# Kernel optimization log

Hardware: AMD Instinct MI355X
Metric: run time of the kernel (lower is better)

Reference implementation:

```python
import jax, jax.numpy as jnp
import numpy as np

H_SIZE, Z_SIZE, A_SIZE, INTER = 50, 100, 2, 100
T = 16384
SLOPE = 0.01  # torch leaky_relu default


def _lrelu(x):
    return jnp.where(x >= 0, x, SLOPE * x)


def setup_inputs() -> dict:
    key = jax.random.key(0)
    ks = jax.random.split(key, 20)
    s = 0.05
    inp = {
        "z_seq": jax.random.normal(ks[0], (T, 1, Z_SIZE), jnp.float32),
        "a_seq": jax.random.normal(ks[1], (T, 1, A_SIZE), jnp.float32),
        "term_seq": jax.random.uniform(ks[2], (T, 1, 1), jnp.float32),
        "W1": jax.random.normal(ks[3], (100, Z_SIZE + A_SIZE)) * s,
        "b1": jnp.zeros((100,), jnp.float32),
        "W2": jax.random.normal(ks[4], (INTER, 100)) * s,
        "b2": jnp.zeros((INTER,), jnp.float32),
        "W3": jax.random.normal(ks[5], (100, INTER)) * s,
        "b3": jnp.zeros((100,), jnp.float32),
        "W4": jax.random.normal(ks[6], (H_SIZE, 100)) * s,
        "b4": jnp.zeros((H_SIZE,), jnp.float32),
        "W5": jax.random.normal(ks[7], (100, INTER + H_SIZE)) * s,
        "b5": jnp.zeros((100,), jnp.float32),
        "Wz": jax.random.normal(ks[8], (Z_SIZE, 100)) * s,
        "bz": jnp.zeros((Z_SIZE,), jnp.float32),
        "Wt": jax.random.normal(ks[9], (1, 100)) * s,
        "bt": jnp.zeros((1,), jnp.float32),
    }
    return inp


def reference(z_seq, a_seq, term_seq, W1, b1, W2, b2, W3, b3, W4, b4, W5, b5, Wz, bz, Wt, bt):
    def step(h, xs):
        a, z, z_next, term_next = xs  # a:[1,2] z:[1,100] term_next:[1,1]
        # encode_az
        az = jnp.concatenate([a, z], axis=1)  # [1,102]
        inter = _lrelu(az @ W1.T + b1)
        inter = _lrelu(inter @ W2.T + b2)
        # update_h (residual)
        h = h + (_lrelu(inter @ W3.T + b3) @ W4.T + b4)
        # predict_output
        inp = jnp.concatenate([h, inter], axis=1)  # [1,150]
        i5 = _lrelu(inp @ W5.T + b5)
        z_pred = i5 @ Wz.T + bz
        t_logit = i5 @ Wt.T + bt
        z_loss = jnp.mean((z_next - z_pred) ** 2)
        # BCE with logits (stable)
        t_loss = jnp.mean(jnp.maximum(t_logit, 0) - t_logit * term_next
                          + jnp.log1p(jnp.exp(-jnp.abs(t_logit))))
        return h, (z_loss, t_loss)

    h0 = jnp.zeros((1, H_SIZE), z_seq.dtype)
    _, (zl, tl) = jax.lax.scan(
        step, h0, (a_seq[:-1], z_seq[:-1], z_seq[1:], term_seq[1:]))
    z_loss = jnp.mean(zl)
    term_loss = jnp.mean(tl)
    return (z_loss + term_loss, z_loss, term_loss)
```

## Files before the change

kernel.cpp:

```cpp
#include <hip/hip_runtime.h>
#include <math.h>

#define NS   16383
#define NSP  16384
#define LPB  32
#define NBLK 512
#define TPB  512

#define OFF_INTR 0
#define OFF_DELT (OFF_INTR + 1048576)
#define OFF_CSUM (OFF_DELT + 819200)
#define OFF_BZ   (OFF_CSUM + 50*NBLK)
#define OFF_BT   (OFF_BZ + NBLK)
#define OFF_PACK (OFF_BT + NBLK)

#define PK1 0
#define PK2 16384
#define PK3 32768
#define PK4 49152
#define PK5 57344
#define PKZ 81920
#define PKTOT 98304

using bf16x8 = __attribute__((ext_vector_type(8))) short;
using f32x4  = __attribute__((ext_vector_type(4))) float;

__device__ __forceinline__ unsigned short f2bf(float f) {
    unsigned int x = __float_as_uint(f);
    return (unsigned short)((x + 0x7fffu + ((x >> 16) & 1u)) >> 16);
}
__device__ __forceinline__ float bf2f(unsigned short u) {
    return __uint_as_float(((unsigned int)u) << 16);
}
__device__ __forceinline__ float lrelu(float x) { return fmaxf(x, 0.01f * x); }

__device__ __forceinline__ bf16x8 ldA(const unsigned short* buf, int strideSh, int row, int kc) {
    const int idx = (row * strideSh + kc) ^ ((row & 7) << 3);
    return *(const bf16x8*)(buf + idx);
}
__device__ __forceinline__ bf16x8 ldB(const unsigned short* pk, int KS, int nt, int ks, int lane) {
    return *(const bf16x8*)(pk + (size_t)(((nt * KS + ks) << 6) + lane) * 8);
}
__device__ __forceinline__ f32x4 MF(bf16x8 a, bf16x8 b, f32x4 c) {
    return __builtin_amdgcn_mfma_f32_16x16x32_bf16(a, b, c, 0, 0, 0);
}

#define MLAYER(INBUF, PKOFF, KSN, BIAS, OUTBUF)                                 \
    {                                                                           \
        const int nn = w * 16 + rl;                                             \
        const float bv = (nn < 100) ? (BIAS)[nn] : 0.f;                         \
        bf16x8 bfr[KSN];                                                        \
        _Pragma("unroll")                                                       \
        for (int ks = 0; ks < (KSN); ++ks)                                      \
            bfr[ks] = ldB(packw + (PKOFF), KSN, w, ks, lane);                   \
        _Pragma("unroll")                                                       \
        for (int m = 0; m < 2; ++m) {                                           \
            f32x4 acc; acc.x = bv; acc.y = bv; acc.z = bv; acc.w = bv;          \
            _Pragma("unroll")                                                   \
            for (int ks = 0; ks < (KSN); ++ks)                                  \
                acc = MF(ldA(INBUF, 128, m * 16 + rl, ks * 32 + g8), bfr[ks], acc); \
            _Pragma("unroll")                                                   \
            for (int r = 0; r < 4; ++r) {                                       \
                const int row = m * 16 + dr + r;                                \
                (OUTBUF)[((row << 7) + nn) ^ ((row & 7) << 3)] = f2bf(lrelu(acc[r])); \
            }                                                                   \
        }                                                                       \
    }

__global__ __launch_bounds__(256)
void k0_pack(const float* __restrict__ W1, const float* __restrict__ W2,
             const float* __restrict__ W3, const float* __restrict__ W4,
             const float* __restrict__ W5, const float* __restrict__ Wz,
             float* __restrict__ ws)
{
    const int idx = blockIdx.x * 256 + threadIdx.x;
    if (idx >= PKTOT) return;
    int e, KS, layer;
    if      (idx < PK2) { layer = 1; e = idx - PK1; KS = 4; }
    else if (idx < PK3) { layer = 2; e = idx - PK2; KS = 4; }
    else if (idx < PK4) { layer = 3; e = idx - PK3; KS = 4; }
    else if (idx < PK5) { layer = 4; e = idx - PK4; KS = 4; }
    else if (idx < PKZ) { layer = 5; e = idx - PK5; KS = 6; }
    else                { layer = 6; e = idx - PKZ; KS = 4; }
    const int j    = e & 7;
    const int ln   = (e >> 3) & 63;
    const int rest = e >> 9;
    const int ks   = rest % KS;
    const int nt   = rest / KS;
    const int n    = nt * 16 + (ln & 15);
    const int k    = ks * 32 + ((ln >> 4) << 3) + j;
    float v = 0.f;
    if (layer == 1)      { if (n < 100 && k < 102) v = W1[n * 102 + k]; }
    else if (layer == 2) { if (n < 100 && k < 100) v = W2[n * 100 + k]; }
    else if (layer == 3) { if (n < 100 && k < 100) v = W3[n * 100 + k]; }
    else if (layer == 4) { if (n < 50  && k < 100) v = W4[n * 100 + k]; }
    else if (layer == 5) { if (n < 100) {
                               if (k < 50) v = W5[n * 150 + k];
                               else if (k >= 64 && k < 164) v = W5[n * 150 + k - 14]; } }
    else                 { if (n < 100 && k < 100) v = Wz[n * 100 + k]; }
    ((unsigned short*)(ws + OFF_PACK))[idx] = f2bf(v);
}

__global__ __launch_bounds__(TPB, 4)
void k1_encode(const float* __restrict__ z_seq, const float* __restrict__ a_seq,
               const float* __restrict__ b1, const float* __restrict__ b2,
               const float* __restrict__ b3, const float* __restrict__ b4,
               float* __restrict__ ws)
{
    __shared__ unsigned short Vp[32 * 128];
    __shared__ unsigned short Vq[32 * 128];
    __shared__ float Dl[32 * 64];

    const int tid  = threadIdx.x;
    const int lane = tid & 63;
    const int w    = __builtin_amdgcn_readfirstlane(tid >> 6);
    const int blk  = blockIdx.x;
    const int t0   = blk * LPB;

    const unsigned short* packw = (const unsigned short*)(ws + OFF_PACK);
    unsigned int* interR = (unsigned int*)(ws + OFF_INTR);
    float* deltaT = ws + OFF_DELT;
    float* csum   = ws + OFF_CSUM;

    if (tid < 32) {
        const int t = tid;
        const float a0 = a_seq[(t0 + t) * 2 + 0];
        const float a1 = a_seq[(t0 + t) * 2 + 1];
        *(unsigned int*)&Vp[((t << 7) + 0) ^ ((t & 7) << 3)] =
            (unsigned int)f2bf(a0) | ((unsigned int)f2bf(a1) << 16);
    }
    for (int i = tid; i < 1600; i += TPB) {
        const int t = i / 50, p = i - t * 50;
        const float2 z2 = *(const float2*)(z_seq + (size_t)(t0 + t) * 100 + 2 * p);
        *(unsigned int*)&Vp[((t << 7) + 2 + 2 * p) ^ ((t & 7) << 3)] =
            (unsigned int)f2bf(z2.x) | ((unsigned int)f2bf(z2.y) << 16);
    }
    for (int i = tid; i < 416; i += TPB) {
        const int t = i / 13, p = i - t * 13;
        *(unsigned int*)&Vp[((t << 7) + 102 + 2 * p) ^ ((t & 7) << 3)] = 0u;
    }
    __syncthreads();

    const int rl = lane & 15;
    const int g8 = (lane >> 4) << 3;
    const int dr = (lane >> 4) << 2;

    MLAYER(Vp, PK1, 4, b1, Vq);
    __syncthreads();
    MLAYER(Vq, PK2, 4, b2, Vp);
    __syncthreads();
    for (int i = tid; i < 2048; i += TPB) {
        const int t = i >> 6, c2 = i & 63;
        interR[(size_t)(t0 + t) * 64 + c2] =
            *(const unsigned int*)&Vp[((t << 7) + (c2 << 1)) ^ ((t & 7) << 3)];
    }
    MLAYER(Vp, PK3, 4, b3, Vq);
    __syncthreads();

    if (w < 4) {
        const int nn = w * 16 + rl;
        const float bv = (nn < 50) ? b4[nn] : 0.f;
        bf16x8 bfr[4];
        #pragma unroll
        for (int ks = 0; ks < 4; ++ks) bfr[ks] = ldB(packw + PK4, 4, w, ks, lane);
        #pragma unroll
        for (int m = 0; m < 2; ++m) {
            f32x4 acc; acc.x = bv; acc.y = bv; acc.z = bv; acc.w = bv;
            #pragma unroll
            for (int ks = 0; ks < 4; ++ks)
                acc = MF(ldA(Vq, 128, m * 16 + rl, ks * 32 + g8), bfr[ks], acc);
            #pragma unroll
            for (int r = 0; r < 4; ++r) {
                const int row = m * 16 + dr + r;
                Dl[row * 64 + (nn ^ row)] = acc[r];
            }
        }
    }
    __syncthreads();

    for (int i = tid; i < 1600; i += TPB) {
        const int n = i >> 5, l = i & 31;
        float v = Dl[l * 64 + (n ^ l)];
        if (t0 + l >= NS) v = 0.f;
        deltaT[n * NSP + t0 + l] = v;
        float s = v;
        #pragma unroll
        for (int off = 16; off > 0; off >>= 1) s += __shfl_xor(s, off, 32);
        if ((lane & 31) == 0) csum[n * NBLK + blk] = s;
    }
}

__global__ __launch_bounds__(TPB, 4)
void k3_predict(const float* __restrict__ z_seq, const float* __restrict__ term_seq,
                const float* __restrict__ b5, const float* __restrict__ bz,
                const float* __restrict__ Wt, const float* __restrict__ bt,
                float* __restrict__ ws)
{
    __shared__ unsigned short Ib[32 * 128];
    __shared__ unsigned short I5[32 * 128];
    __shared__ unsigned short ZN[32 * 128];
    __shared__ unsigned short Hb[32 * 64];
    __shared__ float Dl[32 * 64];
    __shared__ float redz[8];

    const int tid  = threadIdx.x;
    const int lane = tid & 63;
    const int w    = __builtin_amdgcn_readfirstlane(tid >> 6);
    const int blk  = blockIdx.x;
    const int t0   = blk * LPB;

    const unsigned short* packw = (const unsigned short*)(ws + OFF_PACK);
    const unsigned int* interR = (const unsigned int*)(ws + OFF_INTR);
    const float* deltaT = ws + OFF_DELT;
    const float* csum   = ws + OFF_CSUM;
    float* g_bz = ws + OFF_BZ;
    float* g_bt = ws + OFF_BT;

    for (int i = tid; i < 2048; i += TPB) {
        const int t = i >> 6, c2 = i & 63;
        *(unsigned int*)&Ib[((t << 7) + (c2 << 1)) ^ ((t & 7) << 3)] =
            interR[(size_t)(t0 + t) * 64 + c2];
    }
    for (int i = tid; i < 1600; i += TPB) {
        const int n = i >> 5, l = i & 31;
        Dl[l * 64 + (n ^ l)] = deltaT[n * NSP + t0 + l];
    }
    for (int i = tid; i < 1600; i += TPB) {
        const int t = i / 50, p = i - t * 50;
        int t1 = t0 + t + 1; t1 = t1 > NS ? NS : t1;
        const float2 z2 = *(const float2*)(z_seq + (size_t)t1 * 100 + 2 * p);
        *(unsigned int*)&ZN[((t << 7) + 2 * p) ^ ((t & 7) << 3)] =
            (unsigned int)f2bf(z2.x) | ((unsigned int)f2bf(z2.y) << 16);
    }
    for (int i = tid; i < 224; i += TPB) {
        const int t = i / 7, p = i - t * 7;
        *(unsigned int*)&Hb[((t << 6) + 50 + 2 * p) ^ ((t & 7) << 3)] = 0u;
    }
    __syncthreads();

    for (int pass = 0; pass < 4; ++pass) {
        const int n = pass * 16 + w * 2 + (lane >> 5);
        if (n < 50) {
            const int sl = lane & 31;
            float s = 0.f;
            #pragma unroll
            for (int i2 = 0; i2 < 4; ++i2) {
                const int c0 = (sl + (i2 << 5)) << 2;
                if (c0 < blk) {
                    const f32x4 v4 = *(const f32x4*)(csum + n * NBLK + c0);
                    #pragma unroll
                    for (int e = 0; e < 4; ++e)
                        if (c0 + e < blk) s += v4[e];
                }
            }
            #pragma unroll
            for (int off = 16; off > 0; off >>= 1) s += __shfl_xor(s, off, 32);
            float v = Dl[sl * 64 + (n ^ sl)];
            #pragma unroll
            for (int off = 1; off < 32; off <<= 1) {
                const float u = __shfl_up(v, off, 32);
                if (sl >= off) v += u;
            }
            Hb[((sl << 6) + n) ^ ((sl & 7) << 3)] = f2bf(v + s);
        }
    }
    __syncthreads();

    const int rl = lane & 15;
    const int g8 = (lane >> 4) << 3;
    const int dr = (lane >> 4) << 2;

    {
        const int nn = w * 16 + rl;
        const float bv = (nn < 100) ? b5[nn] : 0.f;
        bf16x8 bfr[6];
        #pragma unroll
        for (int ks = 0; ks < 6; ++ks) bfr[ks] = ldB(packw + PK5, 6, w, ks, lane);
        #pragma unroll
        for (int m = 0; m < 2; ++m) {
            f32x4 acc; acc.x = bv; acc.y = bv; acc.z = bv; acc.w = bv;
            #pragma unroll
            for (int ks = 0; ks < 6; ++ks) {
                const bf16x8 a = (ks < 2) ? ldA(Hb, 64, m * 16 + rl, ks * 32 + g8)
                                          : ldA(Ib, 128, m * 16 + rl, (ks - 2) * 32 + g8);
                acc = MF(a, bfr[ks], acc);
            }
            #pragma unroll
            for (int r = 0; r < 4; ++r) {
                const int row = m * 16 + dr + r;
                I5[((row << 7) + nn) ^ ((row & 7) << 3)] = f2bf(lrelu(acc[r]));
            }
        }
    }
    __syncthreads();

    float zpart = 0.f;
    {
        const int nn = w * 16 + rl;
        const float bv = (nn < 100) ? bz[nn] : 0.f;
        bf16x8 bfr[4];
        #pragma unroll
        for (int ks = 0; ks < 4; ++ks) bfr[ks] = ldB(packw + PKZ, 4, w, ks, lane);
        #pragma unroll
        for (int m = 0; m < 2; ++m) {
            f32x4 acc; acc.x = bv; acc.y = bv; acc.z = bv; acc.w = bv;
            #pragma unroll
            for (int ks = 0; ks < 4; ++ks)
                acc = MF(ldA(I5, 128, m * 16 + rl, ks * 32 + g8), bfr[ks], acc);
            if (nn < 100) {
                #pragma unroll
                for (int r = 0; r < 4; ++r) {
                    const int row = m * 16 + dr + r;
                    if (t0 + row < NS) {
                        const float zn = bf2f(ZN[((row << 7) + nn) ^ ((row & 7) << 3)]);
                        const float d = zn - acc[r];
                        zpart += d * d;
                    }
                }
            }
        }
    }

    float tpart = 0.f;
    if (w == 0 && lane < 32) {
        const bool vl = (t0 + lane) < NS;
        float a = bt[0];
        #pragma unroll
        for (int g = 0; g < 13; ++g) {
            const bf16x8 v = *(const bf16x8*)(I5 + (((lane << 7) + 8 * g) ^ ((lane & 7) << 3)));
            #pragma unroll
            for (int j = 0; j < 8; ++j) {
                const int c = 8 * g + j;
                if (c < 100) a = fmaf(bf2f((unsigned short)v[j]), Wt[c], a);
            }
        }
        if (vl) {
            const float y = term_seq[t0 + lane + 1];
            tpart = fmaxf(a, 0.f) - a * y + log1pf(expf(-fabsf(a)));
        }
    }

    #pragma unroll
    for (int off = 32; off > 0; off >>= 1) zpart += __shfl_xor(zpart, off, 64);
    if (lane == 0) redz[w] = zpart;
    __syncthreads();
    if (tid == 0) {
        float s = 0.f;
        #pragma unroll
        for (int i = 0; i < 8; ++i) s += redz[i];
        g_bz[blk] = s;
    }
    if (w == 0) {
        #pragma unroll
        for (int off = 16; off > 0; off >>= 1) tpart += __shfl_xor(tpart, off, 32);
        if (lane == 0) g_bt[blk] = tpart;
    }
}

__global__ __launch_bounds__(512)
void k4_final(const float* __restrict__ ws, float* __restrict__ out)
{
    __shared__ float rz[8], rt[8];
    const float* g_bz = ws + OFF_BZ;
    const float* g_bt = ws + OFF_BT;
    const int tid  = threadIdx.x;
    const int lane = tid & 63;
    const int w    = tid >> 6;
    float z = g_bz[tid];
    float t = g_bt[tid];
    #pragma unroll
    for (int off = 32; off > 0; off >>= 1) {
        z += __shfl_xor(z, off, 64);
        t += __shfl_xor(t, off, 64);
    }
    if (lane == 0) { rz[w] = z; rt[w] = t; }
    __syncthreads();
    if (tid == 0) {
        float sz = 0.f, st = 0.f;
        #pragma unroll
        for (int i = 0; i < 8; ++i) { sz += rz[i]; st += rt[i]; }
        const float zl = sz / (100.0f * NS);
        const float tl = st / NS;
        out[0] = zl + tl;
        out[1] = zl;
        out[2] = tl;
    }
}

extern "C" void kernel_launch(void* const* d_in, const int* in_sizes, int n_in,
                              void* d_out, int out_size, void* d_ws, size_t ws_size,
                              hipStream_t stream)
{
    const float* z_seq = (const float*)d_in[0];
    const float* a_seq = (const float*)d_in[1];
    const float* term  = (const float*)d_in[2];
    const float* W1 = (const float*)d_in[3];  const float* b1 = (const float*)d_in[4];
    const float* W2 = (const float*)d_in[5];  const float* b2 = (const float*)d_in[6];
    const float* W3 = (const float*)d_in[7];  const float* b3 = (const float*)d_in[8];
    const float* W4 = (const float*)d_in[9];  const float* b4 = (const float*)d_in[10];
    const float* W5 = (const float*)d_in[11]; const float* b5 = (const float*)d_in[12];
    const float* Wz = (const float*)d_in[13]; const float* bz = (const float*)d_in[14];
    const float* Wt = (const float*)d_in[15]; const float* bt = (const float*)d_in[16];
    float* out = (float*)d_out;
    float* ws  = (float*)d_ws;

    k0_pack<<<384, 256, 0, stream>>>(W1, W2, W3, W4, W5, Wz, ws);
    k1_encode<<<NBLK, TPB, 0, stream>>>(z_seq, a_seq, b1, b2, b3, b4, ws);
    k3_predict<<<NBLK, TPB, 0, stream>>>(z_seq, term, b5, bz, Wt, bt, ws);
    k4_final<<<1, 512, 0, stream>>>(ws, out);
}
```

Before: 31.89 us.

## Fold weight packing into encode kernel and read z_next directly from global

Removes the separate packing kernel. The encode layers now load their weights straight from the fp32 matrices and convert them to bf16 in registers. Extra blocks appended to the encode launch pack only the W5 and Wz fragments that the predict kernel still needs. The predict kernel also drops the shared-memory ZN staging and reads the next-step z directly from global memory in fp32. This saves one launch and a staging pass, at the cost of redundant per-block weight conversion and uncoalesced strided global reads in the z-loss loop.

```diff
diff --git a/kernel.cpp b/kernel.cpp
--- a/kernel.cpp
+++ b/kernel.cpp
@@ -1,4 +1,5 @@
 #include <hip/hip_runtime.h>
+#include <hip/hip_bf16.h>
 #include <math.h>
 
 #define NS   16383
@@ -6,6 +7,7 @@
 #define LPB  32
 #define NBLK 512
 #define TPB  512
+#define PACKBLK 80
 
 #define OFF_INTR 0
 #define OFF_DELT (OFF_INTR + 1048576)
@@ -14,10 +16,6 @@
 #define OFF_BT   (OFF_BZ + NBLK)
 #define OFF_PACK (OFF_BT + NBLK)
 
-#define PK1 0
-#define PK2 16384
-#define PK3 32768
-#define PK4 49152
 #define PK5 57344
 #define PKZ 81920
 #define PKTOT 98304
@@ -41,23 +39,58 @@
 __device__ __forceinline__ bf16x8 ldB(const unsigned short* pk, int KS, int nt, int ks, int lane) {
     return *(const bf16x8*)(pk + (size_t)(((nt * KS + ks) << 6) + lane) * 8);
 }
+__device__ __forceinline__ bf16x8 loadW(const float* __restrict__ W, const int Kst,
+                                        const int klim, const int Nmax,
+                                        const int n, const int kbase) {
+    const bool nv = (n < Nmax);
+    const int nc = nv ? n : (Nmax - 1);
+    const float* p = W + (size_t)nc * Kst + kbase;
+    float f[8];
+    if (kbase + 7 < klim) {
+        if ((Kst & 3) == 0) {
+            const float4 a = *(const float4*)p;
+            const float4 b = *(const float4*)(p + 4);
+            f[0]=a.x; f[1]=a.y; f[2]=a.z; f[3]=a.w;
+            f[4]=b.x; f[5]=b.y; f[6]=b.z; f[7]=b.w;
+        } else {
+            #pragma unroll
+            for (int q = 0; q < 4; ++q) {
+                const float2 t2 = *(const float2*)(p + 2 * q);
+                f[2*q] = t2.x; f[2*q+1] = t2.y;
+            }
+        }
+    } else {
+        #pragma unroll
+        for (int j = 0; j < 8; ++j) f[j] = (kbase + j < klim) ? p[j] : 0.f;
+    }
+    union { bf16x8 v; unsigned int u[4]; } r;
+    #pragma unroll
+    for (int q = 0; q < 4; ++q) {
+        const float lo = nv ? f[2*q]   : 0.f;
+        const float hi = nv ? f[2*q+1] : 0.f;
+        const __hip_bfloat162 b2 = __float22bfloat162_rn(make_float2(lo, hi));
+        unsigned int uu; __builtin_memcpy(&uu, &b2, 4);
+        r.u[q] = uu;
+    }
+    return r.v;
+}
 __device__ __forceinline__ f32x4 MF(bf16x8 a, bf16x8 b, f32x4 c) {
     return __builtin_amdgcn_mfma_f32_16x16x32_bf16(a, b, c, 0, 0, 0);
 }
 
-#define MLAYER(INBUF, PKOFF, KSN, BIAS, OUTBUF)                                 \
+#define DLAYER(INBUF, WPTR, KST, KLIM, BIAS, OUTBUF)                            \
     {                                                                           \
         const int nn = w * 16 + rl;                                             \
         const float bv = (nn < 100) ? (BIAS)[nn] : 0.f;                         \
-        bf16x8 bfr[KSN];                                                        \
+        bf16x8 bfr[4];                                                          \
         _Pragma("unroll")                                                       \
-        for (int ks = 0; ks < (KSN); ++ks)                                      \
-            bfr[ks] = ldB(packw + (PKOFF), KSN, w, ks, lane);                   \
+        for (int ks = 0; ks < 4; ++ks)                                          \
+            bfr[ks] = loadW(WPTR, KST, KLIM, 100, nn, ks * 32 + g8);            \
         _Pragma("unroll")                                                       \
         for (int m = 0; m < 2; ++m) {                                           \
             f32x4 acc; acc.x = bv; acc.y = bv; acc.z = bv; acc.w = bv;          \
             _Pragma("unroll")                                                   \
-            for (int ks = 0; ks < (KSN); ++ks)                                  \
+            for (int ks = 0; ks < 4; ++ks)                                      \
                 acc = MF(ldA(INBUF, 128, m * 16 + rl, ks * 32 + g8), bfr[ks], acc); \
             _Pragma("unroll")                                                   \
             for (int r = 0; r < 4; ++r) {                                       \
@@ -67,57 +100,47 @@
         }                                                                       \
     }
 
-__global__ __launch_bounds__(256)
-void k0_pack(const float* __restrict__ W1, const float* __restrict__ W2,
-             const float* __restrict__ W3, const float* __restrict__ W4,
-             const float* __restrict__ W5, const float* __restrict__ Wz,
-             float* __restrict__ ws)
-{
-    const int idx = blockIdx.x * 256 + threadIdx.x;
-    if (idx >= PKTOT) return;
-    int e, KS, layer;
-    if      (idx < PK2) { layer = 1; e = idx - PK1; KS = 4; }
-    else if (idx < PK3) { layer = 2; e = idx - PK2; KS = 4; }
-    else if (idx < PK4) { layer = 3; e = idx - PK3; KS = 4; }
-    else if (idx < PK5) { layer = 4; e = idx - PK4; KS = 4; }
-    else if (idx < PKZ) { layer = 5; e = idx - PK5; KS = 6; }
-    else                { layer = 6; e = idx - PKZ; KS = 4; }
-    const int j    = e & 7;
-    const int ln   = (e >> 3) & 63;
-    const int rest = e >> 9;
-    const int ks   = rest % KS;
-    const int nt   = rest / KS;
-    const int n    = nt * 16 + (ln & 15);
-    const int k    = ks * 32 + ((ln >> 4) << 3) + j;
-    float v = 0.f;
-    if (layer == 1)      { if (n < 100 && k < 102) v = W1[n * 102 + k]; }
-    else if (layer == 2) { if (n < 100 && k < 100) v = W2[n * 100 + k]; }
-    else if (layer == 3) { if (n < 100 && k < 100) v = W3[n * 100 + k]; }
-    else if (layer == 4) { if (n < 50  && k < 100) v = W4[n * 100 + k]; }
-    else if (layer == 5) { if (n < 100) {
-                               if (k < 50) v = W5[n * 150 + k];
-                               else if (k >= 64 && k < 164) v = W5[n * 150 + k - 14]; } }
-    else                 { if (n < 100 && k < 100) v = Wz[n * 100 + k]; }
-    ((unsigned short*)(ws + OFF_PACK))[idx] = f2bf(v);
-}
-
 __global__ __launch_bounds__(TPB, 4)
 void k1_encode(const float* __restrict__ z_seq, const float* __restrict__ a_seq,
-               const float* __restrict__ b1, const float* __restrict__ b2,
-               const float* __restrict__ b3, const float* __restrict__ b4,
+               const float* __restrict__ W1, const float* __restrict__ b1,
+               const float* __restrict__ W2, const float* __restrict__ b2,
+               const float* __restrict__ W3, const float* __restrict__ b3,
+               const float* __restrict__ W4, const float* __restrict__ b4,
+               const float* __restrict__ W5, const float* __restrict__ Wz,
                float* __restrict__ ws)
 {
+    const int blk = blockIdx.x;
+    const int tid = threadIdx.x;
+
+    if (blk >= NBLK) {
+        const int idx = PK5 + (blk - NBLK) * TPB + tid;
+        int e, KS, layer;
+        if (idx < PKZ) { layer = 5; e = idx - PK5; KS = 6; }
+        else           { layer = 6; e = idx - PKZ; KS = 4; }
+        const int j    = e & 7;
+        const int ln   = (e >> 3) & 63;
+        const int rest = e >> 9;
+        const int ks   = rest % KS;
+        const int nt   = rest / KS;
+        const int n    = nt * 16 + (ln & 15);
+        const int k    = ks * 32 + ((ln >> 4) << 3) + j;
+        float v = 0.f;
+        if (layer == 5) { if (n < 100) {
+                              if (k < 50) v = W5[n * 150 + k];
+                              else if (k >= 64 && k < 164) v = W5[n * 150 + k - 14]; } }
+        else            { if (n < 100 && k < 100) v = Wz[n * 100 + k]; }
+        ((unsigned short*)(ws + OFF_PACK))[idx] = f2bf(v);
+        return;
+    }
+
     __shared__ unsigned short Vp[32 * 128];
     __shared__ unsigned short Vq[32 * 128];
     __shared__ float Dl[32 * 64];
 
-    const int tid  = threadIdx.x;
     const int lane = tid & 63;
     const int w    = __builtin_amdgcn_readfirstlane(tid >> 6);
-    const int blk  = blockIdx.x;
     const int t0   = blk * LPB;
 
-    const unsigned short* packw = (const unsigned short*)(ws + OFF_PACK);
     unsigned int* interR = (unsigned int*)(ws + OFF_INTR);
     float* deltaT = ws + OFF_DELT;
     float* csum   = ws + OFF_CSUM;
@@ -145,16 +168,16 @@
     const int g8 = (lane >> 4) << 3;
     const int dr = (lane >> 4) << 2;
 
-    MLAYER(Vp, PK1, 4, b1, Vq);
-    __syncthreads();
-    MLAYER(Vq, PK2, 4, b2, Vp);
+    DLAYER(Vp, W1, 102, 102, b1, Vq);
+    __syncthreads();
+    DLAYER(Vq, W2, 100, 100, b2, Vp);
     __syncthreads();
     for (int i = tid; i < 2048; i += TPB) {
         const int t = i >> 6, c2 = i & 63;
         interR[(size_t)(t0 + t) * 64 + c2] =
             *(const unsigned int*)&Vp[((t << 7) + (c2 << 1)) ^ ((t & 7) << 3)];
     }
-    MLAYER(Vp, PK3, 4, b3, Vq);
+    DLAYER(Vp, W3, 100, 100, b3, Vq);
     __syncthreads();
 
     if (w < 4) {
@@ -162,7 +185,8 @@
         const float bv = (nn < 50) ? b4[nn] : 0.f;
         bf16x8 bfr[4];
         #pragma unroll
-        for (int ks = 0; ks < 4; ++ks) bfr[ks] = ldB(packw + PK4, 4, w, ks, lane);
+        for (int ks = 0; ks < 4; ++ks)
+            bfr[ks] = loadW(W4, 100, 100, 50, nn, ks * 32 + g8);
         #pragma unroll
         for (int m = 0; m < 2; ++m) {
             f32x4 acc; acc.x = bv; acc.y = bv; acc.z = bv; acc.w = bv;
@@ -198,7 +222,6 @@
 {
     __shared__ unsigned short Ib[32 * 128];
     __shared__ unsigned short I5[32 * 128];
-    __shared__ unsigned short ZN[32 * 128];
     __shared__ unsigned short Hb[32 * 64];
     __shared__ float Dl[32 * 64];
     __shared__ float redz[8];
@@ -224,13 +247,6 @@
     for (int i = tid; i < 1600; i += TPB) {
         const int n = i >> 5, l = i & 31;
         Dl[l * 64 + (n ^ l)] = deltaT[n * NSP + t0 + l];
-    }
-    for (int i = tid; i < 1600; i += TPB) {
-        const int t = i / 50, p = i - t * 50;
-        int t1 = t0 + t + 1; t1 = t1 > NS ? NS : t1;
-        const float2 z2 = *(const float2*)(z_seq + (size_t)t1 * 100 + 2 * p);
-        *(unsigned int*)&ZN[((t << 7) + 2 * p) ^ ((t & 7) << 3)] =
-            (unsigned int)f2bf(z2.x) | ((unsigned int)f2bf(z2.y) << 16);
     }
     for (int i = tid; i < 224; i += TPB) {
         const int t = i / 7, p = i - t * 7;
@@ -312,7 +328,7 @@
                 for (int r = 0; r < 4; ++r) {
                     const int row = m * 16 + dr + r;
                     if (t0 + row < NS) {
-                        const float zn = bf2f(ZN[((row << 7) + nn) ^ ((row & 7) << 3)]);
+                        const float zn = z_seq[(size_t)(t0 + row + 1) * 100 + nn];
                         const float d = zn - acc[r];
                         zpart += d * d;
                     }
@@ -404,8 +420,8 @@
     float* out = (float*)d_out;
     float* ws  = (float*)d_ws;
 
-    k0_pack<<<384, 256, 0, stream>>>(W1, W2, W3, W4, W5, Wz, ws);
-    k1_encode<<<NBLK, TPB, 0, stream>>>(z_seq, a_seq, b1, b2, b3, b4, ws);
+    k1_encode<<<NBLK + PACKBLK, TPB, 0, stream>>>(z_seq, a_seq, W1, b1, W2, b2,
+                                                  W3, b3, W4, b4, W5, Wz, ws);
     k3_predict<<<NBLK, TPB, 0, stream>>>(z_seq, term, b5, bz, Wt, bt, ws);
     k4_final<<<1, 512, 0, stream>>>(ws, out);
 }
```

After: 32.66 us. 2.4% more time.
